# Kernel optimization log

Hardware: AMD Instinct MI355X
Metric: run time of the kernel (lower is better)

The kernel has to match this reference:

```python
import jax, jax.numpy as jnp
import numpy as np

B, N, M = 4, 4096, 4096  # samples, pred pts/sample, target pts/sample
LOSS_WEIGHT = 1.0


def setup_inputs() -> dict:
    key = jax.random.key(0)
    k1, k2, k3 = jax.random.split(key, 3)
    pred_pc = jax.random.normal(k1, (B * N, 3), dtype=jnp.float32)
    target = jax.random.normal(k2, (B * M, 3), dtype=jnp.float32)
    label = jax.random.randint(k3, (B * N,), 0, 2)  # binary keep-mask per pred point
    nums = jnp.full((B,), N, dtype=jnp.int32)        # uniform ragged sizes (static for jit)
    dense_nums = jnp.full((B,), M, dtype=jnp.int32)
    return {"pred_pc": pred_pc, "target": target, "label": label,
            "nums": nums, "dense_nums": dense_nums}


def reference(pred_pc, target, label, nums, dense_nums):
    b = nums.shape[0]
    p = pred_pc.reshape(b, -1, 3)      # [B,N,3]
    t = target.reshape(b, -1, 3)       # [B,M,3]
    mask = (label.reshape(b, -1) == 1) # [B,N] valid pred points

    # squared pairwise distances via |p|^2 + |t|^2 - 2 p.t  -> [B,N,M]
    pn = jnp.sum(p * p, axis=-1)
    tn = jnp.sum(t * t, axis=-1)
    d = pn[:, :, None] + tn[:, None, :] - 2.0 * jnp.einsum('bnd,bmd->bnm', p, t)
    d = jnp.maximum(d, 0.0)

    # pred -> target: min over M, L1 (sqrt before mean), masked mean over valid preds
    d1 = jnp.sqrt(jnp.min(d, axis=2))                              # [B,N]
    cnt = jnp.maximum(jnp.sum(mask, axis=1), 1)
    m1 = jnp.sum(jnp.where(mask, d1, 0.0), axis=1) / cnt           # [B]

    # target -> pred: min over valid pred points only (invalid rows masked to +big)
    BIG = jnp.float32(1e10)
    d2 = jnp.sqrt(jnp.min(jnp.where(mask[:, :, None], d, BIG), axis=1))  # [B,M]
    m2 = jnp.mean(d2, axis=1)                                      # [B]

    per_sample = 0.5 * (m1 + m2)   # ChamferDistanceL1: (d1.mean()+d2.mean())/2
    return jnp.mean(per_sample) * LOSS_WEIGHT
```

## Files before the change

kernel.cpp:

```cpp
#include <hip/hip_runtime.h>

#define TPB   128
#define QPT   8
#define SPLIT 32
#define RTPB  256

__global__ void __launch_bounds__(TPB) nn_kernel(
    const float* __restrict__ pred,
    const float* __restrict__ target,
    const int*   __restrict__ label,
    float* __restrict__ minsplit,
    int B, int N, int M, int natmax, int stride)
{
    __shared__ float4 tile[TPB];

    const int dir = blockIdx.z;
    const float* __restrict__ A  = dir ? target : pred;
    const float* __restrict__ Bp = dir ? pred   : target;
    const int NA = dir ? M : N;
    const int NB = dir ? N : M;
    const int* __restrict__ labB = dir ? label : nullptr;

    const int natiles = (NA + TPB * QPT - 1) / (TPB * QPT);
    const int b  = blockIdx.x / natmax;
    const int at = blockIdx.x - b * natmax;
    if (at >= natiles) return;

    const size_t abase = (size_t)b * NA;

    float px[QPT], py[QPT], pz[QPT], pn[QPT], best[QPT];
#pragma unroll
    for (int q = 0; q < QPT; ++q) {
        int a = at * (TPB * QPT) + q * TPB + threadIdx.x;
        int idx = (a < NA) ? a : 0;
        const float* sp = A + (abase + idx) * 3;
        px[q] = sp[0];
        py[q] = sp[1];
        pz[q] = sp[2];
        pn[q] = fmaf(px[q], px[q], fmaf(py[q], py[q], pz[q] * pz[q]));
        best[q] = 3.0e38f;
    }

    const int slen = (NB + SPLIT - 1) / SPLIT;
    const int sbeg = blockIdx.y * slen;
    const int send = min(sbeg + slen, NB);
    const size_t bbase = (size_t)b * NB;

    for (int c = sbeg; c < send; c += TPB) {
        int m = c + threadIdx.x;
        float4 qv = make_float4(0.0f, 0.0f, 0.0f, 1.0e10f);
        if (m < send) {
            const float* sp = Bp + (bbase + m) * 3;
            float x = sp[0], y = sp[1], z = sp[2];
            float tn = fmaf(x, x, fmaf(y, y, z * z));
            if (labB != nullptr && labB[bbase + m] != 1) {
                x = 0.0f; y = 0.0f; z = 0.0f; tn = 1.0e10f;
            }
            qv = make_float4(x, y, z, tn);
        }
        __syncthreads();
        tile[threadIdx.x] = qv;
        __syncthreads();

        const int jn = min(send - c, TPB);
        const int jeven = jn & ~1;
#pragma unroll 8
        for (int j = 0; j < jeven; j += 2) {
            float4 t0 = tile[j];
            float4 t1 = tile[j + 1];
#pragma unroll
            for (int q = 0; q < QPT; ++q) {
                float s0 = fmaf(px[q], t0.x, fmaf(py[q], t0.y, pz[q] * t0.z));
                float s1 = fmaf(px[q], t1.x, fmaf(py[q], t1.y, pz[q] * t1.z));
                float v0 = fmaf(-2.0f, s0, t0.w);
                float v1 = fmaf(-2.0f, s1, t1.w);
                best[q] = fminf(best[q], fminf(v0, v1));
            }
        }
        if (jn & 1) {
            float4 t0 = tile[jn - 1];
#pragma unroll
            for (int q = 0; q < QPT; ++q) {
                float s0 = fmaf(px[q], t0.x, fmaf(py[q], t0.y, pz[q] * t0.z));
                best[q] = fminf(best[q], fmaf(-2.0f, s0, t0.w));
            }
        }
    }

    float* out = minsplit + (((size_t)dir * B + b) * SPLIT + blockIdx.y) * stride;
#pragma unroll
    for (int q = 0; q < QPT; ++q) {
        int a = at * (TPB * QPT) + q * TPB + threadIdx.x;
        if (a < NA) {
            out[a] = fmaxf(best[q] + pn[q], 0.0f);
        }
    }
}

__device__ float block_reduce_sum(float v, float* red) {
    int tid = threadIdx.x;
    red[tid] = v;
    __syncthreads();
    for (int s = RTPB / 2; s > 0; s >>= 1) {
        if (tid < s) red[tid] += red[tid + s];
        __syncthreads();
    }
    float r = red[0];
    __syncthreads();
    return r;
}

__global__ void __launch_bounds__(RTPB) partial_kernel(
    const float* __restrict__ minsplit,
    const int* __restrict__ label,
    float* __restrict__ s1, float* __restrict__ c1, float* __restrict__ s2,
    int B, int N, int M, int ptN, int ptM, int stride)
{
    __shared__ float red[RTPB];
    const int r = blockIdx.x;
    const int regionN = B * ptN;

    if (r < regionN) {
        int b = r / ptN;
        int t = r - b * ptN;
        int n = t * RTPB + threadIdx.x;
        float s = 0.0f, cc = 0.0f;
        if (n < N) {
            const float* base = minsplit + ((size_t)b * SPLIT) * stride + n;
            float m = base[0];
            for (int sp = 1; sp < SPLIT; ++sp) {
                m = fminf(m, base[(size_t)sp * stride]);
            }
            if (label[(size_t)b * N + n] == 1) {
                s = sqrtf(m);
                cc = 1.0f;
            }
        }
        s  = block_reduce_sum(s, red);
        cc = block_reduce_sum(cc, red);
        if (threadIdx.x == 0) { s1[r] = s; c1[r] = cc; }
    } else {
        int r2 = r - regionN;
        int b = r2 / ptM;
        int t = r2 - b * ptM;
        int mq = t * RTPB + threadIdx.x;
        float s = 0.0f;
        if (mq < M) {
            const float* base = minsplit + (((size_t)B + b) * SPLIT) * stride + mq;
            float m = base[0];
            for (int sp = 1; sp < SPLIT; ++sp) {
                m = fminf(m, base[(size_t)sp * stride]);
            }
            s = sqrtf(m);
        }
        s = block_reduce_sum(s, red);
        if (threadIdx.x == 0) s2[r2] = s;
    }
}

__global__ void __launch_bounds__(64) final_kernel(
    const float* __restrict__ s1, const float* __restrict__ c1,
    const float* __restrict__ s2,
    float* __restrict__ out, int B, int M, int ptN, int ptM)
{
    __shared__ float acc[64];
    int tid = threadIdx.x;
    float v = 0.0f;
    if (tid < B) {
        float S1 = 0.0f, C1 = 0.0f, S2 = 0.0f;
        for (int i = 0; i < ptN; ++i) { S1 += s1[tid * ptN + i]; C1 += c1[tid * ptN + i]; }
        for (int i = 0; i < ptM; ++i) { S2 += s2[tid * ptM + i]; }
        float m1 = S1 / fmaxf(C1, 1.0f);
        float m2 = S2 / (float)M;
        v = 0.5f * (m1 + m2);
    }
    acc[tid] = v;
    __syncthreads();
    if (tid == 0) {
        float a = 0.0f;
        for (int b = 0; b < B; ++b) a += acc[b];
        out[0] = a / (float)B;
    }
}

extern "C" void kernel_launch(void* const* d_in, const int* in_sizes, int n_in,
                              void* d_out, int out_size, void* d_ws, size_t ws_size,
                              hipStream_t stream) {
    const float* pred   = (const float*)d_in[0];
    const float* target = (const float*)d_in[1];
    const int*   label  = (const int*)  d_in[2];

    const int B = in_sizes[3];
    const int N = in_sizes[2] / B;
    const int M = in_sizes[1] / (3 * B);

    const int stride = (N > M) ? N : M;

    float* minsplit = (float*)d_ws;
    const int ptN = (N + RTPB - 1) / RTPB;
    const int ptM = (M + RTPB - 1) / RTPB;
    float* s1 = minsplit + (size_t)2 * B * SPLIT * stride;
    float* c1 = s1 + (size_t)B * ptN;
    float* s2 = c1 + (size_t)B * ptN;

    const int nat1 = (N + TPB * QPT - 1) / (TPB * QPT);
    const int nat2 = (M + TPB * QPT - 1) / (TPB * QPT);
    const int natmax = (nat1 > nat2) ? nat1 : nat2;
    dim3 g(B * natmax, SPLIT, 2);
    nn_kernel<<<g, TPB, 0, stream>>>(pred, target, label, minsplit,
                                     B, N, M, natmax, stride);

    const int nred = B * (ptN + ptM);
    partial_kernel<<<nred, RTPB, 0, stream>>>(minsplit, label, s1, c1, s2,
                                              B, N, M, ptN, ptM, stride);

    final_kernel<<<1, 64, 0, stream>>>(s1, c1, s2, (float*)d_out, B, M, ptN, ptM);
}
```

Measured before the change: 35.58 us.

## Fold -2 scale into tile, fuse final reduction via last-block atomic counter

Pre-scales the staged target coordinates by -2 so each distance costs three FMAs instead of four operations, and adds a full-tile fast path with a fixed trip count. The partial and final reduction kernels are merged into one kernel whose last block, detected with an atomic counter reset by the NN kernel, computes the scalar loss. That removes one launch. Each thread now reduces four points with float4 loads. Occupancy is hinted through launch_bounds.

```diff
diff --git a/kernel.cpp b/kernel.cpp
--- a/kernel.cpp
+++ b/kernel.cpp
@@ -4,15 +4,21 @@
 #define QPT   8
 #define SPLIT 32
 #define RTPB  256
-
-__global__ void __launch_bounds__(TPB) nn_kernel(
+#define QPR   4
+
+__global__ void __launch_bounds__(TPB, 4) nn_kernel(
     const float* __restrict__ pred,
     const float* __restrict__ target,
     const int*   __restrict__ label,
     float* __restrict__ minsplit,
+    unsigned int* __restrict__ counter,
     int B, int N, int M, int natmax, int stride)
 {
     __shared__ float4 tile[TPB];
+
+    if (blockIdx.x == 0 && blockIdx.y == 0 && blockIdx.z == 0 && threadIdx.x == 0) {
+        *counter = 0u;
+    }
 
     const int dir = blockIdx.z;
     const float* __restrict__ A  = dir ? target : pred;
@@ -56,33 +62,33 @@
             if (labB != nullptr && labB[bbase + m] != 1) {
                 x = 0.0f; y = 0.0f; z = 0.0f; tn = 1.0e10f;
             }
-            qv = make_float4(x, y, z, tn);
+            qv = make_float4(-2.0f * x, -2.0f * y, -2.0f * z, tn);
         }
         __syncthreads();
         tile[threadIdx.x] = qv;
         __syncthreads();
 
-        const int jn = min(send - c, TPB);
-        const int jeven = jn & ~1;
+        if (send - c >= TPB) {
 #pragma unroll 8
-        for (int j = 0; j < jeven; j += 2) {
-            float4 t0 = tile[j];
-            float4 t1 = tile[j + 1];
-#pragma unroll
-            for (int q = 0; q < QPT; ++q) {
-                float s0 = fmaf(px[q], t0.x, fmaf(py[q], t0.y, pz[q] * t0.z));
-                float s1 = fmaf(px[q], t1.x, fmaf(py[q], t1.y, pz[q] * t1.z));
-                float v0 = fmaf(-2.0f, s0, t0.w);
-                float v1 = fmaf(-2.0f, s1, t1.w);
-                best[q] = fminf(best[q], fminf(v0, v1));
-            }
-        }
-        if (jn & 1) {
-            float4 t0 = tile[jn - 1];
-#pragma unroll
-            for (int q = 0; q < QPT; ++q) {
-                float s0 = fmaf(px[q], t0.x, fmaf(py[q], t0.y, pz[q] * t0.z));
-                best[q] = fminf(best[q], fmaf(-2.0f, s0, t0.w));
+            for (int j = 0; j < TPB; j += 2) {
+                float4 t0 = tile[j];
+                float4 t1 = tile[j + 1];
+#pragma unroll
+                for (int q = 0; q < QPT; ++q) {
+                    float v0 = fmaf(px[q], t0.x, fmaf(py[q], t0.y, fmaf(pz[q], t0.z, t0.w)));
+                    float v1 = fmaf(px[q], t1.x, fmaf(py[q], t1.y, fmaf(pz[q], t1.z, t1.w)));
+                    best[q] = fminf(best[q], fminf(v0, v1));
+                }
+            }
+        } else {
+            int jn = send - c;
+            for (int j = 0; j < jn; ++j) {
+                float4 t0 = tile[j];
+#pragma unroll
+                for (int q = 0; q < QPT; ++q) {
+                    float v0 = fmaf(px[q], t0.x, fmaf(py[q], t0.y, fmaf(pz[q], t0.z, t0.w)));
+                    best[q] = fminf(best[q], v0);
+                }
             }
         }
     }
@@ -97,7 +103,7 @@
     }
 }
 
-__device__ float block_reduce_sum(float v, float* red) {
+__device__ __forceinline__ float block_reduce_sum(float v, float* red) {
     int tid = threadIdx.x;
     red[tid] = v;
     __syncthreads();
@@ -110,76 +116,86 @@
     return r;
 }
 
-__global__ void __launch_bounds__(RTPB) partial_kernel(
+__global__ void __launch_bounds__(RTPB) reduce_kernel(
     const float* __restrict__ minsplit,
     const int* __restrict__ label,
-    float* __restrict__ s1, float* __restrict__ c1, float* __restrict__ s2,
-    int B, int N, int M, int ptN, int ptM, int stride)
+    float* __restrict__ pS, float* __restrict__ pC,
+    unsigned int* __restrict__ counter,
+    float* __restrict__ out,
+    int B, int N, int M, int tilesN, int tilesM, int stride, int nblocks)
 {
     __shared__ float red[RTPB];
     const int r = blockIdx.x;
-    const int regionN = B * ptN;
-
-    if (r < regionN) {
-        int b = r / ptN;
-        int t = r - b * ptN;
-        int n = t * RTPB + threadIdx.x;
-        float s = 0.0f, cc = 0.0f;
-        if (n < N) {
-            const float* base = minsplit + ((size_t)b * SPLIT) * stride + n;
-            float m = base[0];
-            for (int sp = 1; sp < SPLIT; ++sp) {
-                m = fminf(m, base[(size_t)sp * stride]);
-            }
-            if (label[(size_t)b * N + n] == 1) {
-                s = sqrtf(m);
-                cc = 1.0f;
-            }
-        }
-        s  = block_reduce_sum(s, red);
-        cc = block_reduce_sum(cc, red);
-        if (threadIdx.x == 0) { s1[r] = s; c1[r] = cc; }
+
+    int dir, b, t, NA;
+    if (r < B * tilesN) { dir = 0; b = r / tilesN; t = r - b * tilesN; NA = N; }
+    else { int r2 = r - B * tilesN; dir = 1; b = r2 / tilesM; t = r2 - b * tilesM; NA = M; }
+
+    const float* base = minsplit + (((size_t)dir * B + b) * SPLIT) * stride;
+    const int q0 = t * (RTPB * QPR) + threadIdx.x * QPR;
+
+    float s = 0.0f, cc = 0.0f;
+    if (q0 + QPR <= NA) {
+        float4 mv = *reinterpret_cast<const float4*>(base + q0);
+#pragma unroll 8
+        for (int sp = 1; sp < SPLIT; ++sp) {
+            float4 v = *reinterpret_cast<const float4*>(base + (size_t)sp * stride + q0);
+            mv.x = fminf(mv.x, v.x);
+            mv.y = fminf(mv.y, v.y);
+            mv.z = fminf(mv.z, v.z);
+            mv.w = fminf(mv.w, v.w);
+        }
+        if (dir == 0) {
+            int4 lb = *reinterpret_cast<const int4*>(label + (size_t)b * N + q0);
+            if (lb.x == 1) { s += sqrtf(mv.x); cc += 1.0f; }
+            if (lb.y == 1) { s += sqrtf(mv.y); cc += 1.0f; }
+            if (lb.z == 1) { s += sqrtf(mv.z); cc += 1.0f; }
+            if (lb.w == 1) { s += sqrtf(mv.w); cc += 1.0f; }
+        } else {
+            s = sqrtf(mv.x) + sqrtf(mv.y) + sqrtf(mv.z) + sqrtf(mv.w);
+        }
     } else {
-        int r2 = r - regionN;
-        int b = r2 / ptM;
-        int t = r2 - b * ptM;
-        int mq = t * RTPB + threadIdx.x;
-        float s = 0.0f;
-        if (mq < M) {
-            const float* base = minsplit + (((size_t)B + b) * SPLIT) * stride + mq;
-            float m = base[0];
-            for (int sp = 1; sp < SPLIT; ++sp) {
-                m = fminf(m, base[(size_t)sp * stride]);
-            }
-            s = sqrtf(m);
-        }
-        s = block_reduce_sum(s, red);
-        if (threadIdx.x == 0) s2[r2] = s;
-    }
-}
-
-__global__ void __launch_bounds__(64) final_kernel(
-    const float* __restrict__ s1, const float* __restrict__ c1,
-    const float* __restrict__ s2,
-    float* __restrict__ out, int B, int M, int ptN, int ptM)
-{
-    __shared__ float acc[64];
-    int tid = threadIdx.x;
-    float v = 0.0f;
-    if (tid < B) {
-        float S1 = 0.0f, C1 = 0.0f, S2 = 0.0f;
-        for (int i = 0; i < ptN; ++i) { S1 += s1[tid * ptN + i]; C1 += c1[tid * ptN + i]; }
-        for (int i = 0; i < ptM; ++i) { S2 += s2[tid * ptM + i]; }
-        float m1 = S1 / fmaxf(C1, 1.0f);
-        float m2 = S2 / (float)M;
-        v = 0.5f * (m1 + m2);
-    }
-    acc[tid] = v;
-    __syncthreads();
-    if (tid == 0) {
-        float a = 0.0f;
-        for (int b = 0; b < B; ++b) a += acc[b];
-        out[0] = a / (float)B;
+        for (int k = 0; k < QPR; ++k) {
+            int q = q0 + k;
+            if (q < NA) {
+                float m = base[q];
+                for (int sp = 1; sp < SPLIT; ++sp) {
+                    m = fminf(m, base[(size_t)sp * stride + q]);
+                }
+                if (dir == 0) {
+                    if (label[(size_t)b * N + q] == 1) { s += sqrtf(m); cc += 1.0f; }
+                } else {
+                    s += sqrtf(m);
+                }
+            }
+        }
+    }
+
+    s = block_reduce_sum(s, red);
+    if (dir == 0) cc = block_reduce_sum(cc, red);
+
+    if (threadIdx.x == 0) {
+        atomicExch(&pS[r], s);
+        atomicExch(&pC[r], cc);
+        __threadfence();
+        unsigned int old = atomicAdd(counter, 1u);
+        if (old == (unsigned int)(nblocks - 1)) {
+            float acc = 0.0f;
+            for (int bb = 0; bb < B; ++bb) {
+                float S1 = 0.0f, C1 = 0.0f, S2 = 0.0f;
+                for (int i = 0; i < tilesN; ++i) {
+                    S1 += atomicAdd(&pS[bb * tilesN + i], 0.0f);
+                    C1 += atomicAdd(&pC[bb * tilesN + i], 0.0f);
+                }
+                for (int i = 0; i < tilesM; ++i) {
+                    S2 += atomicAdd(&pS[B * tilesN + bb * tilesM + i], 0.0f);
+                }
+                float m1 = S1 / fmaxf(C1, 1.0f);
+                float m2 = S2 / (float)M;
+                acc += 0.5f * (m1 + m2);
+            }
+            out[0] = acc / (float)B;
+        }
     }
 }
 
@@ -197,22 +213,21 @@
     const int stride = (N > M) ? N : M;
 
     float* minsplit = (float*)d_ws;
-    const int ptN = (N + RTPB - 1) / RTPB;
-    const int ptM = (M + RTPB - 1) / RTPB;
-    float* s1 = minsplit + (size_t)2 * B * SPLIT * stride;
-    float* c1 = s1 + (size_t)B * ptN;
-    float* s2 = c1 + (size_t)B * ptN;
+    const int tilesN = (N + RTPB * QPR - 1) / (RTPB * QPR);
+    const int tilesM = (M + RTPB * QPR - 1) / (RTPB * QPR);
+    const int nred = B * (tilesN + tilesM);
+    float* pS = minsplit + (size_t)2 * B * SPLIT * stride;
+    float* pC = pS + nred;
+    unsigned int* counter = (unsigned int*)(pC + nred);
 
     const int nat1 = (N + TPB * QPT - 1) / (TPB * QPT);
     const int nat2 = (M + TPB * QPT - 1) / (TPB * QPT);
     const int natmax = (nat1 > nat2) ? nat1 : nat2;
     dim3 g(B * natmax, SPLIT, 2);
-    nn_kernel<<<g, TPB, 0, stream>>>(pred, target, label, minsplit,
+    nn_kernel<<<g, TPB, 0, stream>>>(pred, target, label, minsplit, counter,
                                      B, N, M, natmax, stride);
 
-    const int nred = B * (ptN + ptM);
-    partial_kernel<<<nred, RTPB, 0, stream>>>(minsplit, label, s1, c1, s2,
-                                              B, N, M, ptN, ptM, stride);
-
-    final_kernel<<<1, 64, 0, stream>>>(s1, c1, s2, (float*)d_out, B, M, ptN, ptM);
-}
+    reduce_kernel<<<nred, RTPB, 0, stream>>>(minsplit, label, pS, pC, counter,
+                                             (float*)d_out,
+                                             B, N, M, tilesN, tilesM, stride, nred);
+}
```

New measurement: 40.97 us. +15.1%, slower.
